# Performance work log

Measured on AMD Instinct MI355X. Metric: run time of the kernel, lower is better.

## Reference

```python
import jax, jax.numpy as jnp
import numpy as np

CHANNELS = 25
BN_EPS = 1e-5


def _diff(x):
    # x: [B,H,W]; zero-pad by 1 on H and W, then shifted slices (same as torch diff())
    xp = jnp.pad(x, ((0, 0), (1, 1), (1, 1)))
    p_x = (xp[:, 2:, 1:-1] - xp[:, :-2, 1:-1]) / 2
    p_y = (xp[:, 1:-1, 2:] - xp[:, 1:-1, :-2]) / 2
    pp_x = xp[:, 2:, 1:-1] + xp[:, :-2, 1:-1] - 2 * x
    pp_y = xp[:, 1:-1, 2:] + xp[:, 1:-1, :-2] - 2 * x
    pp_xy = xp[:, 2:, 2:] + xp[:, :-2, :-2] - xp[:, 2:, 1:-1] - xp[:, 1:-1, 2:]
    return p_x, p_y, pp_x, pp_y, pp_xy


def _batchnorm(x, gamma, beta):
    # x: [B,C,H,W]; training-mode BN with batch statistics (biased variance)
    mean = jnp.mean(x, axis=(0, 2, 3), keepdims=True)
    var = jnp.mean((x - mean) ** 2, axis=(0, 2, 3), keepdims=True)
    xhat = (x - mean) * jax.lax.rsqrt(var + BN_EPS)
    return xhat * gamma[None, :, None, None] + beta[None, :, None, None]


def setup_inputs() -> dict:
    key = jax.random.key(0)
    ks = jax.random.split(key, 5)
    B, H, W = 32, 512, 512
    x = jax.random.normal(ks[0], (B, H, W), dtype=jnp.float32)
    # 1x1 conv weights stored as [out_ch, in_ch]
    w1 = jax.random.normal(ks[1], (CHANNELS, 6), dtype=jnp.float32) * (1.0 / np.sqrt(6.0))
    b1 = jnp.zeros((CHANNELS,), dtype=jnp.float32)
    g1 = jnp.ones((CHANNELS,), dtype=jnp.float32)
    beta1 = jnp.zeros((CHANNELS,), dtype=jnp.float32)
    w2 = jax.random.normal(ks[2], (1, CHANNELS), dtype=jnp.float32) * (1.0 / np.sqrt(CHANNELS))
    b2 = jnp.zeros((1,), dtype=jnp.float32)
    g2 = jnp.ones((1,), dtype=jnp.float32)
    beta2 = jnp.zeros((1,), dtype=jnp.float32)
    return {"x": x, "w1": w1, "b1": b1, "g1": g1, "beta1": beta1,
            "w2": w2, "b2": b2, "g2": g2, "beta2": beta2}


def reference(x, w1, b1, g1, beta1, w2, b2, g2, beta2):
    p_x, p_y, pp_x, pp_y, pp_xy = _diff(x)
    xx = jnp.stack([x, p_x, p_y, pp_x, pp_y, pp_xy], axis=1)  # [B,6,H,W]
    # 1x1 conv == per-pixel channel matmul
    h = jnp.einsum('bchw,oc->bohw', xx, w1) + b1[None, :, None, None]
    h = jax.nn.relu(_batchnorm(h, g1, beta1))  # [B,25,H,W]
    o = jnp.einsum('bchw,oc->bohw', h, w2) + b2[None, :, None, None]
    o = jax.nn.relu(_batchnorm(o, g2, beta2))[:, 0, :, :]  # [B,H,W]
    return o + x
```

## Files before the change

### kernel.cpp

```cpp
#include <hip/hip_runtime.h>
#include <hip/hip_fp16.h>

typedef float f4 __attribute__((ext_vector_type(4)));
typedef float f2 __attribute__((ext_vector_type(2)));
typedef _Float16 f16x8 __attribute__((ext_vector_type(8)));
typedef float f32x16 __attribute__((ext_vector_type(16)));

#define NPIX (32*512*512)
#define BN_EPS 1e-5f


__global__ __launch_bounds__(256) void k_moments(const float* __restrict__ x,
                                                 const float* __restrict__ ws,
                                                 float* __restrict__ outp) {
    __shared__ ushort sl[4][8][64];
    __shared__ float mom[4][7][7];
    int t = threadIdx.x;
    int l = t & 63, wv = t >> 6;
    int h = l >> 5;
    const float* zb = ws + 1024;

    sl[wv][6][l] = (ushort)0x3C00;
    sl[wv][7][l] = (ushort)0;

    f32x16 accA, accB;
    #pragma unroll
    for (int r = 0; r < 16; ++r) { accA[r] = 0.f; accB[r] = 0.f; }

    int arow = ((l & 31) < 7) ? (l & 31) : 7;
    const ushort* rdp = &sl[wv][arow][8*h];

    int wave_id = blockIdx.x * 4 + wv;
    #pragma unroll 1
    for (int rr = 0; rr < 2; ++rr) {
        int row = wave_id * 2 + rr;
        int i = row & 511;
        const float* xr = x + row * 512;
        const float* xn = (i > 0)   ? xr - 512 : zb;
        const float* xs = (i < 511) ? xr + 512 : zb;
        #pragma unroll 1
        for (int it = 0; it < 8; ++it) {
            int col = it * 64 + l;
            bool okw = (col > 0), oke = (col < 511);
            int cm = okw ? col - 1 : 0;
            int cp = oke ? col + 1 : 511;
            float C  = xr[col], N = xn[col], S_ = xs[col];
            float W_ = xr[cm],  E = xr[cp];
            float NW = xn[cm],  SE = xs[cp];
            W_ = okw ? W_ : 0.f; NW = okw ? NW : 0.f;
            E  = oke ? E  : 0.f; SE = oke ? SE : 0.f;

            float s0 = C;
            float s1 = (S_ - N) * 0.5f;
            float s2 = (E - W_) * 0.5f;
            float s3 = S_ + N - 2.f*C;
            float s4 = E + W_ - 2.f*C;
            float s5 = SE + NW - S_ - E;

            __half h0 = __float2half(s0), h1 = __float2half(s1);
            __half h2 = __float2half(s2), h3 = __float2half(s3);
            __half h4 = __float2half(s4), h5 = __float2half(s5);
            sl[wv][0][l] = *(ushort*)&h0;
            sl[wv][1][l] = *(ushort*)&h1;
            sl[wv][2][l] = *(ushort*)&h2;
            sl[wv][3][l] = *(ushort*)&h3;
            sl[wv][4][l] = *(ushort*)&h4;
            sl[wv][5][l] = *(ushort*)&h5;
            __builtin_amdgcn_wave_barrier();

            union { uint4 u; f16x8 v; } f0, f1, f2_, f3;
            f0.u  = *(const uint4*)(rdp);
            f1.u  = *(const uint4*)(rdp + 16);
            f2_.u = *(const uint4*)(rdp + 32);
            f3.u  = *(const uint4*)(rdp + 48);
            accA = __builtin_amdgcn_mfma_f32_32x32x16_f16(f0.v,  f0.v,  accA, 0, 0, 0);
            accB = __builtin_amdgcn_mfma_f32_32x32x16_f16(f1.v,  f1.v,  accB, 0, 0, 0);
            accA = __builtin_amdgcn_mfma_f32_32x32x16_f16(f2_.v, f2_.v, accA, 0, 0, 0);
            accB = __builtin_amdgcn_mfma_f32_32x32x16_f16(f3.v,  f3.v,  accB, 0, 0, 0);
            __builtin_amdgcn_wave_barrier();
        }
    }

    if ((l & 31) < 7) {
        int j = l & 31;
        #pragma unroll
        for (int r = 0; r < 4; ++r) {
            int irow = r + 4*h;
            if (irow < 7) mom[wv][irow][j] = accA[r] + accB[r];
        }
    }
    __syncthreads();
    if (t < 27) {
        int a, b;
        if (t < 6) { a = t; b = 6; }
        else {
            int rem = t - 6; a = 0;
            while (rem >= 6 - a) { rem -= 6 - a; ++a; }
            b = a + rem;
        }
        float v = mom[0][a][b] + mom[1][a][b] + mom[2][a][b] + mom[3][a][b];
        outp[t*2048 + blockIdx.x] = v;
    }
}

__global__ __launch_bounds__(256) void k_red(const float* __restrict__ outp,
                                             float* __restrict__ ws) {
    int b = blockIdx.x;
    int t = threadIdx.x;
    float v = 0.f;
    #pragma unroll
    for (int k = 0; k < 8; ++k) v += outp[b*2048 + t + 256*k];
    for (int off = 32; off; off >>= 1) v += __shfl_xor(v, off);
    __shared__ float red[4];
    int wave = t >> 6, lane = t & 63;
    if (lane == 0) red[wave] = v;
    __syncthreads();
    if (t == 0) ws[b] = red[0] + red[1] + red[2] + red[3];
}

__global__ void k_stats1(const float* w1, const float* b1, const float* g1,
                         const float* beta1, const float* w2, float* ws) {
    __shared__ float sm[32][8];
    int c = threadIdx.x;
    if (c < 32) {
        #pragma unroll
        for (int k = 0; k < 8; ++k) sm[c][k] = 0.f;
        ws[64 + c] = (c < 25) ? w2[c] : 0.f;
    }
    __syncthreads();
    if (c < 25) {
        const float invN = 1.f / (float)NPIX;
        float m1[6], wr[6];
        #pragma unroll
        for (int i = 0; i < 6; ++i) m1[i] = ws[i] * invN;
        #pragma unroll
        for (int i = 0; i < 6; ++i) wr[i] = w1[c*6 + i];
        float bc = b1[c];
        float mean = bc;
        #pragma unroll
        for (int i = 0; i < 6; ++i) mean = fmaf(wr[i], m1[i], mean);
        float e2 = bc * bc;
        #pragma unroll
        for (int i = 0; i < 6; ++i) e2 = fmaf(2.f*bc*wr[i], m1[i], e2);
        #pragma unroll
        for (int i = 0; i < 6; ++i)
            #pragma unroll
            for (int j = 0; j < 6; ++j) {
                int a = i < j ? i : j, b = i < j ? j : i;
                float m2 = ws[6 + a*(11-a)/2 + b] * invN;
                e2 = fmaf(wr[i]*wr[j], m2, e2);
            }
        float var = e2 - mean*mean;
        float a1 = g1[c] * rsqrtf(var + BN_EPS);
        #pragma unroll
        for (int i = 0; i < 6; ++i) sm[c][i] = a1 * wr[i];
        sm[c][6] = fmaf(a1, bc - mean, beta1[c]);
    }
    __syncthreads();
    int ch = c & 31, h = c >> 5;
    float aC=0.f, aN=0.f, aS=0.f, aE=0.f, aW=0.f, aNW=0.f, aSE=0.f, ab=0.f;
    if (h == 0) {
        float w0 = sm[ch][0], w1v = sm[ch][1], w2v = sm[ch][2];
        float w3 = sm[ch][3], w4v = sm[ch][4], w5 = sm[ch][5], be = sm[ch][6];
        aC  = w0 - 2.f*w3 - 2.f*w4v;
        aN  = -0.5f*w1v + w3;
        aS  =  0.5f*w1v + w3 - w5;
        aE  =  0.5f*w2v + w4v - w5;
        aW  = -0.5f*w2v + w4v;
        aNW = w5;
        aSE = w5;
        ab  = be;
    }
    __half2 p0 = __floats2half2_rn(aC,  aN);
    __half2 p1 = __floats2half2_rn(aS,  aE);
    __half2 p2 = __floats2half2_rn(aW,  aNW);
    __half2 p3 = __floats2half2_rn(aSE, ab);
    unsigned u0, u1, u2, u3;
    __builtin_memcpy(&u0, &p0, 4);
    __builtin_memcpy(&u1, &p1, 4);
    __builtin_memcpy(&u2, &p2, 4);
    __builtin_memcpy(&u3, &p3, 4);
    uint4 fr = {u0, u1, u2, u3};
    ((uint4*)(ws + 96))[c] = fr;
}

__global__ __launch_bounds__(256) void k_main(const float* __restrict__ x,
                                              const float* __restrict__ ws,
                                              const float* __restrict__ b2,
                                              float* __restrict__ stats,
                                              __half* __restrict__ oph) {
    int t = threadIdx.x;
    int l = t & 63, wv = t >> 6;
    int lane31 = l & 31, h = l >> 5;
    const float* zb = ws + 1024;

    f16x8 afr;
    {
        uint4 u = ((const uint4*)(ws + 96))[l];
        union { uint4 u; f16x8 v; } cv; cv.u = u; afr = cv.v;
    }
    float w2v[16];
    #pragma unroll
    for (int r = 0; r < 16; ++r) {
        int creg = (r & 3) + 8 * (r >> 2);
        w2v[r] = ws[64 + creg + 4*h];
    }
    f32x16 zacc;
    #pragma unroll
    for (int r = 0; r < 16; ++r) zacc[r] = 0.f;
    float b2v = b2[0];
    float S1 = 0.f, S2 = 0.f;

    int wave_id = blockIdx.x * 4 + wv;
    #pragma unroll 1
    for (int rr = 0; rr < 2; ++rr) {
        int row = wave_id * 2 + rr;
        int i = row & 511;
        const float* xc = x + row * 512 + lane31;
        const float* xn = (i > 0)   ? xc - 512 : zb + lane31;
        const float* xs = (i < 511) ? xc + 512 : zb + lane31;
        __half* op = oph + row * 512 + lane31;

        #pragma unroll
        for (int jt = 0; jt < 16; ++jt) {
            const int o4 = jt * 32;
            int offm1 = o4 - 1, offp1 = o4 + 1;
            if (jt == 0  && lane31 == 0)  offm1 = o4;
            if (jt == 15 && lane31 == 31) offp1 = o4;

            float C  = xc[o4];
            float W_ = xc[offm1];
            float E  = xc[offp1];
            float N  = xn[o4];
            float NW = xn[offm1];
            float S_ = xs[o4];
            float SE = xs[offp1];
            if (jt == 0)  { bool ok = (lane31 != 0);  W_ = ok ? W_ : 0.f; NW = ok ? NW : 0.f; }
            if (jt == 15) { bool ok = (lane31 != 31); E  = ok ? E  : 0.f; SE = ok ? SE : 0.f; }

            __half2 p0 = __floats2half2_rn(C,  N);
            __half2 p1 = __floats2half2_rn(S_, E);
            __half2 p2 = __floats2half2_rn(W_, NW);
            __half2 p3 = __floats2half2_rn(SE, 1.f);
            unsigned u0, u1, u2, u3;
            __builtin_memcpy(&u0, &p0, 4);
            __builtin_memcpy(&u1, &p1, 4);
            __builtin_memcpy(&u2, &p2, 4);
            __builtin_memcpy(&u3, &p3, 4);
            union { uint4 u; f16x8 v; } bv;
            bv.u = (uint4){u0, u1, u2, u3};

            f32x16 acc = __builtin_amdgcn_mfma_f32_32x32x16_f16(afr, bv.v, zacc, 0, 0, 0);

            float o = 0.f;
            #pragma unroll
            for (int r = 0; r < 16; ++r)
                o = fmaf(fmaxf(acc[r], 0.f), w2v[r], o);
            o += __shfl_xor(o, 32);
            o += b2v;
            S1 += o;
            S2 = fmaf(o, o, S2);
            if (l < 32) op[o4] = __float2half(o);
        }
    }

    for (int off = 32; off; off >>= 1) { S1 += __shfl_xor(S1, off); S2 += __shfl_xor(S2, off); }
    __shared__ float red[2][4];
    if (l == 0) { red[0][wv] = S1; red[1][wv] = S2; }
    __syncthreads();
    if (t == 0) stats[2048 + blockIdx.x] = 0.5f*(red[0][0]+red[0][1]+red[0][2]+red[0][3]);
    if (t == 1) stats[4096 + blockIdx.x] = 0.5f*(red[1][0]+red[1][1]+red[1][2]+red[1][3]);
}

__global__ __launch_bounds__(256) void k_redS(float* __restrict__ ws) {
    int t = threadIdx.x;
    float s1 = 0.f, s2 = 0.f;
    #pragma unroll
    for (int k = 0; k < 8; ++k) {
        s1 += ws[2048 + t + 256*k];
        s2 += ws[4096 + t + 256*k];
    }
    for (int off = 32; off; off >>= 1) { s1 += __shfl_xor(s1, off); s2 += __shfl_xor(s2, off); }
    __shared__ float red[2][4];
    int wave = t >> 6, lane = t & 63;
    if (lane == 0) { red[0][wave] = s1; red[1][wave] = s2; }
    __syncthreads();
    if (t == 0) ws[27] = red[0][0] + red[0][1] + red[0][2] + red[0][3];
    if (t == 1) ws[28] = red[1][0] + red[1][1] + red[1][2] + red[1][3];
}

__global__ __launch_bounds__(256) void k_final(const float* __restrict__ x,
                                               const float* __restrict__ ws,
                                               const __half* __restrict__ oph,
                                               const float* __restrict__ g2,
                                               const float* __restrict__ beta2,
                                               float* __restrict__ out) {
    const float invN = 1.f / (float)NPIX;
    float mean = ws[27] * invN;
    float var  = ws[28] * invN - mean*mean;
    float a2 = g2[0] * rsqrtf(var + BN_EPS);
    float c2 = fmaf(-mean, a2, beta2[0]);

    int idx = blockIdx.x * 256 + threadIdx.x;
    uint2 u = ((const uint2*)oph)[idx];
    __half2 h01, h23;
    __builtin_memcpy(&h01, &u.x, 4);
    __builtin_memcpy(&h23, &u.y, 4);
    float2 f01 = __half22float2(h01);
    float2 f23 = __half22float2(h23);
    f4 xv = ((const f4*)x)[idx];
    f4 r;
    r.x = fmaxf(fmaf(a2, f01.x, c2), 0.f) + xv.x;
    r.y = fmaxf(fmaf(a2, f01.y, c2), 0.f) + xv.y;
    r.z = fmaxf(fmaf(a2, f23.x, c2), 0.f) + xv.z;
    r.w = fmaxf(fmaf(a2, f23.y, c2), 0.f) + xv.w;
    ((f4*)out)[idx] = r;
}

extern "C" void kernel_launch(void* const* d_in, const int* in_sizes, int n_in,
                              void* d_out, int out_size, void* d_ws, size_t ws_size,
                              hipStream_t stream) {
    const float* x     = (const float*)d_in[0];
    const float* w1    = (const float*)d_in[1];
    const float* b1    = (const float*)d_in[2];
    const float* g1    = (const float*)d_in[3];
    const float* beta1 = (const float*)d_in[4];
    const float* w2    = (const float*)d_in[5];
    const float* b2    = (const float*)d_in[6];
    const float* g2    = (const float*)d_in[7];
    const float* beta2 = (const float*)d_in[8];
    float* out = (float*)d_out;
    float* ws  = (float*)d_ws;
    __half* oph = (__half*)((char*)d_ws + 65536);

    hipMemsetAsync(ws, 0, 8192, stream);
    k_moments<<<2048, 256, 0, stream>>>(x, ws, out);
    k_red    <<<27, 256, 0, stream>>>(out, ws);
    k_stats1 <<<1, 64, 0, stream>>>(w1, b1, g1, beta1, w2, ws);
    k_main   <<<2048, 256, 0, stream>>>(x, ws, b2, ws, oph);
    k_redS   <<<1, 256, 0, stream>>>(ws);
    k_final  <<<8192, 256, 0, stream>>>(x, ws, oph, g2, beta2, out);
}
```

Before: 92.76 us.

## Compute BN1 moments from raw stencil taps with paired-pixel loads

The moments kernel now builds a Gram matrix of the seven raw stencil neighbours plus a constant, not of the six derived features. Each lane handles two adjacent pixels, so neighbour values are shared and loaded as float2, giving fewer global loads and no per-pixel feature arithmetic. k_stats1 folds the stencil-to-feature transform into effective weights before forming mean and variance, and k_main drops the unused padded accumulator channels (13 of 16). Risks are larger LDS tiles, more moment entries to reduce (36 instead of 27), and shifted workspace offsets.

New measurement: 86.97 us. 6.2% less time.

```diff
diff --git a/kernel.cpp b/kernel.cpp
--- a/kernel.cpp
+++ b/kernel.cpp
@@ -13,21 +13,24 @@
 __global__ __launch_bounds__(256) void k_moments(const float* __restrict__ x,
                                                  const float* __restrict__ ws,
                                                  float* __restrict__ outp) {
-    __shared__ ushort sl[4][8][64];
-    __shared__ float mom[4][7][7];
+    __shared__ ushort sl[4][9][136];
+    __shared__ float mom[4][8][8];
     int t = threadIdx.x;
     int l = t & 63, wv = t >> 6;
     int h = l >> 5;
     const float* zb = ws + 1024;
 
-    sl[wv][6][l] = (ushort)0x3C00;
-    sl[wv][7][l] = (ushort)0;
+    sl[wv][7][l]      = (ushort)0x3C00;
+    sl[wv][7][l + 64] = (ushort)0x3C00;
+    sl[wv][8][l]      = (ushort)0;
+    sl[wv][8][l + 64] = (ushort)0;
 
     f32x16 accA, accB;
     #pragma unroll
     for (int r = 0; r < 16; ++r) { accA[r] = 0.f; accB[r] = 0.f; }
 
-    int arow = ((l & 31) < 7) ? (l & 31) : 7;
+    int a31 = l & 31;
+    int arow = (a31 < 8) ? a31 : 8;
     const ushort* rdp = &sl[wv][arow][8*h];
 
     int wave_id = blockIdx.x * 4 + wv;
@@ -39,65 +42,62 @@
         const float* xn = (i > 0)   ? xr - 512 : zb;
         const float* xs = (i < 511) ? xr + 512 : zb;
         #pragma unroll 1
-        for (int it = 0; it < 8; ++it) {
-            int col = it * 64 + l;
-            bool okw = (col > 0), oke = (col < 511);
-            int cm = okw ? col - 1 : 0;
-            int cp = oke ? col + 1 : 511;
-            float C  = xr[col], N = xn[col], S_ = xs[col];
-            float W_ = xr[cm],  E = xr[cp];
-            float NW = xn[cm],  SE = xs[cp];
-            W_ = okw ? W_ : 0.f; NW = okw ? NW : 0.f;
-            E  = oke ? E  : 0.f; SE = oke ? SE : 0.f;
-
-            float s0 = C;
-            float s1 = (S_ - N) * 0.5f;
-            float s2 = (E - W_) * 0.5f;
-            float s3 = S_ + N - 2.f*C;
-            float s4 = E + W_ - 2.f*C;
-            float s5 = SE + NW - S_ - E;
-
-            __half h0 = __float2half(s0), h1 = __float2half(s1);
-            __half h2 = __float2half(s2), h3 = __float2half(s3);
-            __half h4 = __float2half(s4), h5 = __float2half(s5);
-            sl[wv][0][l] = *(ushort*)&h0;
-            sl[wv][1][l] = *(ushort*)&h1;
-            sl[wv][2][l] = *(ushort*)&h2;
-            sl[wv][3][l] = *(ushort*)&h3;
-            sl[wv][4][l] = *(ushort*)&h4;
-            sl[wv][5][l] = *(ushort*)&h5;
+        for (int p4 = 0; p4 < 4; ++p4) {
+            int c0 = p4 * 128 + 2 * l;
+            f2 C  = *(const f2*)(xr + c0);
+            f2 N_ = *(const f2*)(xn + c0);
+            f2 S_ = *(const f2*)(xs + c0);
+            bool okw = (c0 > 0), oke = (c0 < 510);
+            int cm = okw ? c0 - 1 : c0;
+            int cp = oke ? c0 + 2 : c0;
+            float Wlo  = xr[cm];  Wlo  = okw ? Wlo  : 0.f;
+            float Ehi  = xr[cp];  Ehi  = oke ? Ehi  : 0.f;
+            float NWlo = xn[cm];  NWlo = okw ? NWlo : 0.f;
+            float SEhi = xs[cp];  SEhi = oke ? SEhi : 0.f;
+
+            __half2 q0 = __floats2half2_rn(C.x,  C.y);
+            __half2 q1 = __floats2half2_rn(N_.x, N_.y);
+            __half2 q2 = __floats2half2_rn(S_.x, S_.y);
+            __half2 q3 = __floats2half2_rn(C.y,  Ehi);
+            __half2 q4 = __floats2half2_rn(Wlo,  C.x);
+            __half2 q5 = __floats2half2_rn(NWlo, N_.x);
+            __half2 q6 = __floats2half2_rn(S_.y, SEhi);
+            unsigned v0,v1,v2,v3,v4,v5,v6;
+            __builtin_memcpy(&v0,&q0,4); __builtin_memcpy(&v1,&q1,4);
+            __builtin_memcpy(&v2,&q2,4); __builtin_memcpy(&v3,&q3,4);
+            __builtin_memcpy(&v4,&q4,4); __builtin_memcpy(&v5,&q5,4);
+            __builtin_memcpy(&v6,&q6,4);
+            *(unsigned*)&sl[wv][0][2*l] = v0;
+            *(unsigned*)&sl[wv][1][2*l] = v1;
+            *(unsigned*)&sl[wv][2][2*l] = v2;
+            *(unsigned*)&sl[wv][3][2*l] = v3;
+            *(unsigned*)&sl[wv][4][2*l] = v4;
+            *(unsigned*)&sl[wv][5][2*l] = v5;
+            *(unsigned*)&sl[wv][6][2*l] = v6;
             __builtin_amdgcn_wave_barrier();
 
-            union { uint4 u; f16x8 v; } f0, f1, f2_, f3;
-            f0.u  = *(const uint4*)(rdp);
-            f1.u  = *(const uint4*)(rdp + 16);
-            f2_.u = *(const uint4*)(rdp + 32);
-            f3.u  = *(const uint4*)(rdp + 48);
-            accA = __builtin_amdgcn_mfma_f32_32x32x16_f16(f0.v,  f0.v,  accA, 0, 0, 0);
-            accB = __builtin_amdgcn_mfma_f32_32x32x16_f16(f1.v,  f1.v,  accB, 0, 0, 0);
-            accA = __builtin_amdgcn_mfma_f32_32x32x16_f16(f2_.v, f2_.v, accA, 0, 0, 0);
-            accB = __builtin_amdgcn_mfma_f32_32x32x16_f16(f3.v,  f3.v,  accB, 0, 0, 0);
+            #pragma unroll
+            for (int w16 = 0; w16 < 8; w16 += 2) {
+                union { uint4 u; f16x8 v; } fa, fb;
+                fa.u = *(const uint4*)(rdp + w16*16);
+                fb.u = *(const uint4*)(rdp + w16*16 + 16);
+                accA = __builtin_amdgcn_mfma_f32_32x32x16_f16(fa.v, fa.v, accA, 0, 0, 0);
+                accB = __builtin_amdgcn_mfma_f32_32x32x16_f16(fb.v, fb.v, accB, 0, 0, 0);
+            }
             __builtin_amdgcn_wave_barrier();
         }
     }
 
-    if ((l & 31) < 7) {
-        int j = l & 31;
-        #pragma unroll
-        for (int r = 0; r < 4; ++r) {
-            int irow = r + 4*h;
-            if (irow < 7) mom[wv][irow][j] = accA[r] + accB[r];
-        }
-    }
-    __syncthreads();
-    if (t < 27) {
-        int a, b;
-        if (t < 6) { a = t; b = 6; }
-        else {
-            int rem = t - 6; a = 0;
-            while (rem >= 6 - a) { rem -= 6 - a; ++a; }
-            b = a + rem;
-        }
+    if (a31 < 8) {
+        #pragma unroll
+        for (int r = 0; r < 4; ++r)
+            mom[wv][r + 4*h][a31] = accA[r] + accB[r];
+    }
+    __syncthreads();
+    if (t < 36) {
+        int a = 0, rem = t;
+        while (rem >= 8 - a) { rem -= 8 - a; ++a; }
+        int b = a + rem;
         float v = mom[0][a][b] + mom[1][a][b] + mom[2][a][b] + mom[3][a][b];
         outp[t*2048 + blockIdx.x] = v;
     }
@@ -121,55 +121,61 @@
 __global__ void k_stats1(const float* w1, const float* b1, const float* g1,
                          const float* beta1, const float* w2, float* ws) {
     __shared__ float sm[32][8];
+    __shared__ float G[8][8];
     int c = threadIdx.x;
     if (c < 32) {
         #pragma unroll
         for (int k = 0; k < 8; ++k) sm[c][k] = 0.f;
         ws[64 + c] = (c < 25) ? w2[c] : 0.f;
     }
+    if (c < 36) {
+        int a = 0, rem = c;
+        while (rem >= 8 - a) { rem -= 8 - a; ++a; }
+        int b = a + rem;
+        float v = ws[c];
+        G[a][b] = v; G[b][a] = v;
+    }
     __syncthreads();
     if (c < 25) {
         const float invN = 1.f / (float)NPIX;
-        float m1[6], wr[6];
-        #pragma unroll
-        for (int i = 0; i < 6; ++i) m1[i] = ws[i] * invN;
+        float wr[6];
         #pragma unroll
         for (int i = 0; i < 6; ++i) wr[i] = w1[c*6 + i];
         float bc = b1[c];
-        float mean = bc;
-        #pragma unroll
-        for (int i = 0; i < 6; ++i) mean = fmaf(wr[i], m1[i], mean);
-        float e2 = bc * bc;
-        #pragma unroll
-        for (int i = 0; i < 6; ++i) e2 = fmaf(2.f*bc*wr[i], m1[i], e2);
-        #pragma unroll
-        for (int i = 0; i < 6; ++i)
+        float Wt[8];
+        Wt[0] = wr[0] - 2.f*wr[3] - 2.f*wr[4];
+        Wt[1] = -0.5f*wr[1] + wr[3];
+        Wt[2] =  0.5f*wr[1] + wr[3] - wr[5];
+        Wt[3] =  0.5f*wr[2] + wr[4] - wr[5];
+        Wt[4] = -0.5f*wr[2] + wr[4];
+        Wt[5] = wr[5];
+        Wt[6] = wr[5];
+        Wt[7] = bc;
+        float mean = 0.f;
+        #pragma unroll
+        for (int k = 0; k < 8; ++k) mean = fmaf(Wt[k], G[k][7], mean);
+        mean *= invN;
+        float e2 = 0.f;
+        #pragma unroll
+        for (int k = 0; k < 8; ++k) {
+            float rd = 0.f;
             #pragma unroll
-            for (int j = 0; j < 6; ++j) {
-                int a = i < j ? i : j, b = i < j ? j : i;
-                float m2 = ws[6 + a*(11-a)/2 + b] * invN;
-                e2 = fmaf(wr[i]*wr[j], m2, e2);
-            }
+            for (int m = 0; m < 8; ++m) rd = fmaf(Wt[m], G[k][m], rd);
+            e2 = fmaf(Wt[k], rd, e2);
+        }
+        e2 *= invN;
         float var = e2 - mean*mean;
         float a1 = g1[c] * rsqrtf(var + BN_EPS);
         #pragma unroll
-        for (int i = 0; i < 6; ++i) sm[c][i] = a1 * wr[i];
-        sm[c][6] = fmaf(a1, bc - mean, beta1[c]);
+        for (int k = 0; k < 7; ++k) sm[c][k] = a1 * Wt[k];
+        sm[c][7] = fmaf(a1, bc - mean, beta1[c]);
     }
     __syncthreads();
     int ch = c & 31, h = c >> 5;
     float aC=0.f, aN=0.f, aS=0.f, aE=0.f, aW=0.f, aNW=0.f, aSE=0.f, ab=0.f;
     if (h == 0) {
-        float w0 = sm[ch][0], w1v = sm[ch][1], w2v = sm[ch][2];
-        float w3 = sm[ch][3], w4v = sm[ch][4], w5 = sm[ch][5], be = sm[ch][6];
-        aC  = w0 - 2.f*w3 - 2.f*w4v;
-        aN  = -0.5f*w1v + w3;
-        aS  =  0.5f*w1v + w3 - w5;
-        aE  =  0.5f*w2v + w4v - w5;
-        aW  = -0.5f*w2v + w4v;
-        aNW = w5;
-        aSE = w5;
-        ab  = be;
+        aC = sm[ch][0]; aN = sm[ch][1]; aS = sm[ch][2]; aE = sm[ch][3];
+        aW = sm[ch][4]; aNW = sm[ch][5]; aSE = sm[ch][6]; ab = sm[ch][7];
     }
     __half2 p0 = __floats2half2_rn(aC,  aN);
     __half2 p1 = __floats2half2_rn(aS,  aE);
@@ -199,9 +205,9 @@
         uint4 u = ((const uint4*)(ws + 96))[l];
         union { uint4 u; f16x8 v; } cv; cv.u = u; afr = cv.v;
     }
-    float w2v[16];
-    #pragma unroll
-    for (int r = 0; r < 16; ++r) {
+    float w2v[13];
+    #pragma unroll
+    for (int r = 0; r < 13; ++r) {
         int creg = (r & 3) + 8 * (r >> 2);
         w2v[r] = ws[64 + creg + 4*h];
     }
@@ -254,7 +260,7 @@
 
             float o = 0.f;
             #pragma unroll
-            for (int r = 0; r < 16; ++r)
+            for (int r = 0; r < 13; ++r)
                 o = fmaf(fmaxf(acc[r], 0.f), w2v[r], o);
             o += __shfl_xor(o, 32);
             o += b2v;
@@ -285,8 +291,8 @@
     int wave = t >> 6, lane = t & 63;
     if (lane == 0) { red[0][wave] = s1; red[1][wave] = s2; }
     __syncthreads();
-    if (t == 0) ws[27] = red[0][0] + red[0][1] + red[0][2] + red[0][3];
-    if (t == 1) ws[28] = red[1][0] + red[1][1] + red[1][2] + red[1][3];
+    if (t == 0) ws[40] = red[0][0] + red[0][1] + red[0][2] + red[0][3];
+    if (t == 1) ws[41] = red[1][0] + red[1][1] + red[1][2] + red[1][3];
 }
 
 __global__ __launch_bounds__(256) void k_final(const float* __restrict__ x,
@@ -296,8 +302,8 @@
                                                const float* __restrict__ beta2,
                                                float* __restrict__ out) {
     const float invN = 1.f / (float)NPIX;
-    float mean = ws[27] * invN;
-    float var  = ws[28] * invN - mean*mean;
+    float mean = ws[40] * invN;
+    float var  = ws[41] * invN - mean*mean;
     float a2 = g2[0] * rsqrtf(var + BN_EPS);
     float c2 = fmaf(-mean, a2, beta2[0]);
 
@@ -335,7 +341,7 @@
 
     hipMemsetAsync(ws, 0, 8192, stream);
     k_moments<<<2048, 256, 0, stream>>>(x, ws, out);
-    k_red    <<<27, 256, 0, stream>>>(out, ws);
+    k_red    <<<36, 256, 0, stream>>>(out, ws);
     k_stats1 <<<1, 64, 0, stream>>>(w1, b1, g1, beta1, w2, ws);
     k_main   <<<2048, 256, 0, stream>>>(x, ws, b2, ws, oph);
     k_redS   <<<1, 256, 0, stream>>>(ws);
```
